# Kernel tuning notes

Measured on AMD Instinct MI355X. Metric: run time of the kernel, lower is better.

Reference implementation:

```python
import jax, jax.numpy as jnp
import numpy as np

NS = 100000   # state nodes
NM = 50000    # model nodes (== model_node_count == action space)
E = 600000    # edges
D = 128       # feature dim
HORIZON = 8
NEG_SLOPE = 0.2  # GATv2 default leaky_relu slope


def setup_inputs() -> dict:
    key = jax.random.key(0)
    ks = jax.random.split(key, 20)
    s = 1.0 / np.sqrt(D)
    state_features = jax.random.normal(ks[0], (NS, D), dtype=jnp.float32)
    model_features = jax.random.normal(ks[1], (NM, D), dtype=jnp.float32)
    src = jax.random.randint(ks[2], (E,), 0, NS)
    dst = jax.random.randint(ks[3], (E,), 0, NM)
    edge_index = jnp.stack([src, dst]).astype(jnp.int64)
    # GATv2Conv params (heads=1)
    W_l = jax.random.normal(ks[4], (D, D), dtype=jnp.float32) * s   # lin_l (src/state)
    W_r = jax.random.normal(ks[5], (D, D), dtype=jnp.float32) * s   # lin_r (dst/model)
    att = jax.random.normal(ks[6], (D,), dtype=jnp.float32) * s
    conv_bias = jnp.zeros((D,), dtype=jnp.float32)
    # LSTMCell params (torch gate order i,f,g,o)
    lstm_Wih = jax.random.normal(ks[7], (4 * D, D), dtype=jnp.float32) * s
    lstm_Whh = jax.random.normal(ks[8], (4 * D, D), dtype=jnp.float32) * s
    lstm_bih = jnp.zeros((4 * D,), dtype=jnp.float32)
    lstm_bhh = jnp.zeros((4 * D,), dtype=jnp.float32)
    # predictor MLP: Linear(D,D) -> ReLU -> Linear(D, NM)
    pred_W1 = jax.random.normal(ks[9], (D, D), dtype=jnp.float32) * s
    pred_b1 = jnp.zeros((D,), dtype=jnp.float32)
    pred_W2 = jax.random.normal(ks[10], (NM, D), dtype=jnp.float32) * s
    pred_b2 = jnp.zeros((NM,), dtype=jnp.float32)
    # action embedding
    emb = jax.random.normal(ks[11], (NM, D), dtype=jnp.float32)
    return {
        'state_features': state_features, 'model_features': model_features,
        'edge_index': edge_index, 'W_l': W_l, 'W_r': W_r, 'att': att,
        'conv_bias': conv_bias, 'lstm_Wih': lstm_Wih, 'lstm_Whh': lstm_Whh,
        'lstm_bih': lstm_bih, 'lstm_bhh': lstm_bhh, 'pred_W1': pred_W1,
        'pred_b1': pred_b1, 'pred_W2': pred_W2, 'pred_b2': pred_b2, 'emb': emb,
    }


def _gatv2(state_features, model_features, edge_index, W_l, W_r, att, conv_bias):
    src, dst = edge_index[0], edge_index[1]
    x_l = state_features @ W_l.T        # [NS, D]
    x_r = model_features @ W_r.T        # [NM, D]
    # per-edge GATv2 score: a^T LeakyReLU(x_l[src] + x_r[dst])
    z = x_l[src] + x_r[dst]             # [E, D]
    e = jnp.where(z > 0, z, NEG_SLOPE * z) @ att  # [E]
    # scatter-softmax over destination segments
    m = jax.ops.segment_max(e, dst, num_segments=NM)
    ex = jnp.exp(e - m[dst])
    s = jax.ops.segment_sum(ex, dst, num_segments=NM)
    alpha = ex / s[dst]                 # [E]
    out = jax.ops.segment_sum(alpha[:, None] * x_l[src], dst, num_segments=NM)
    return out + conv_bias              # [NM, D]


def reference(state_features, model_features, edge_index, W_l, W_r, att,
              conv_bias, lstm_Wih, lstm_Whh, lstm_bih, lstm_bhh,
              pred_W1, pred_b1, pred_W2, pred_b2, emb):
    updated = _gatv2(state_features, model_features, edge_index, W_l, W_r, att, conv_bias)
    g = updated.mean(axis=0)            # global model feature [D]

    keys = jax.random.split(jax.random.key(42), HORIZON)

    def step(carry, key):
        h, c, inp = carry
        gates = inp @ lstm_Wih.T + lstm_bih + h @ lstm_Whh.T + lstm_bhh
        i, f, gg, o = jnp.split(gates, 4)
        i = jax.nn.sigmoid(i); f = jax.nn.sigmoid(f)
        gg = jnp.tanh(gg); o = jax.nn.sigmoid(o)
        c = f * c + i * gg
        h = o * jnp.tanh(c)
        logits = jax.nn.relu(h @ pred_W1.T + pred_b1) @ pred_W2.T + pred_b2
        action = jax.random.categorical(key, logits)
        log_prob = jax.nn.log_softmax(logits)[action]
        return (h, c, emb[action]), (action, log_prob)

    h0 = jnp.zeros((D,), dtype=state_features.dtype)
    c0 = jnp.zeros((D,), dtype=state_features.dtype)
    (h, c, _), (actions, log_probs) = jax.lax.scan(step, (h0, c0, g), keys)
    return actions, log_probs, h, c
```

## Files before the change

kernel.cpp:

```cpp
#include <hip/hip_runtime.h>

#define D 128

typedef short s16x8 __attribute__((ext_vector_type(8)));
typedef float f32x4 __attribute__((ext_vector_type(4)));


__device__ __forceinline__ unsigned int encf(float f) {
  unsigned int u = __float_as_uint(f);
  return (u & 0x80000000u) ? ~u : (u | 0x80000000u);
}
__device__ __forceinline__ unsigned short f2bf(float f) {
  unsigned int u = __float_as_uint(f);
  u += 0x7FFFu + ((u >> 16) & 1u);
  return (unsigned short)(u >> 16);
}
__device__ __forceinline__ float bf_lo(unsigned int u) {
  return __uint_as_float(u << 16);
}
__device__ __forceinline__ float bf_hi(unsigned int u) {
  return __uint_as_float(u & 0xFFFF0000u);
}

__device__ __forceinline__ void tf2x32(unsigned int k0, unsigned int k1,
                                       unsigned int& x0, unsigned int& x1) {
  unsigned int ks[3] = {k0, k1, k0 ^ k1 ^ 0x1BD11BDAu};
  x0 += ks[0]; x1 += ks[1];
  const unsigned int rotA[4] = {13u, 15u, 26u, 6u};
  const unsigned int rotB[4] = {17u, 29u, 16u, 24u};
#pragma unroll
  for (int g = 0; g < 5; ++g) {
    const unsigned int* rot = (g & 1) ? rotB : rotA;
#pragma unroll
    for (int i = 0; i < 4; ++i) {
      x0 += x1;
      x1 = (x1 << rot[i]) | (x1 >> (32u - rot[i]));
      x1 ^= x0;
    }
    x0 += ks[(g + 1) % 3];
    x1 += ks[(g + 2) % 3] + (unsigned int)(g + 1);
  }
}


__global__ __launch_bounds__(256) void norm_edges(const int* __restrict__ ei,
                                                  int* __restrict__ src32,
                                                  int* __restrict__ dst32,
                                                  int ne, int ns, int nm) {
  __shared__ int is64;
  if (threadIdx.x == 0) {
    int any = 0;
    for (int i = 1; i < 256; i += 2) any |= ei[i];
    is64 = (any == 0);
  }
  __syncthreads();
  int flag = is64;
  for (int i = blockIdx.x * 256 + threadIdx.x; i < ne; i += gridDim.x * 256) {
    int s = flag ? ei[2 * i] : ei[i];
    int d = flag ? ei[2 * ne + 2 * i] : ei[ne + i];
    s = s < 0 ? 0 : (s >= ns ? ns - 1 : s);
    d = d < 0 ? 0 : (d >= nm ? nm - 1 : d);
    src32[i] = s;
    dst32[i] = d;
  }
}


__device__ __forceinline__ int swz(int row, int kb) {
  return row * 256 + (kb ^ ((row & 7) << 4));
}

__global__ __launch_bounds__(256) void gemm_bf16(const float* __restrict__ X,
                                                 const float* __restrict__ W,
                                                 unsigned short* __restrict__ Y,
                                                 int N) {
  __shared__ __align__(16) unsigned short As[128 * 128];
  __shared__ __align__(16) unsigned short Bs[128 * 128];
  const int tid = threadIdx.x;
  const long long r0 = (long long)blockIdx.x * 128;

#pragma unroll 4
  for (int i = 0; i < 16; ++i) {
    int f = i * 256 + tid;
    int row = f >> 5;
    int j = f & 31;
    float4 wv = *(const float4*)(W + row * D + j * 4);
    uint2 wp;
    wp.x = (unsigned int)f2bf(wv.x) | ((unsigned int)f2bf(wv.y) << 16);
    wp.y = (unsigned int)f2bf(wv.z) | ((unsigned int)f2bf(wv.w) << 16);
    *(uint2*)((char*)Bs + swz(row, j * 8)) = wp;
    long long rr = r0 + row;
    if (rr >= N) rr = N - 1;
    float4 xv = *(const float4*)(X + rr * D + j * 4);
    uint2 xp;
    xp.x = (unsigned int)f2bf(xv.x) | ((unsigned int)f2bf(xv.y) << 16);
    xp.y = (unsigned int)f2bf(xv.z) | ((unsigned int)f2bf(xv.w) << 16);
    *(uint2*)((char*)As + swz(row, j * 8)) = xp;
  }
  __syncthreads();

  const int lane = tid & 63;
  const int wid = tid >> 6;
  const int wr = wid >> 1;
  const int wc = wid & 1;
  const int cl = lane & 15;
  const int sub = lane >> 4;

  f32x4 acc[4][4] = {};

#pragma unroll
  for (int ks = 0; ks < 4; ++ks) {
    s16x8 av[4], bv[4];
#pragma unroll
    for (int m = 0; m < 4; ++m)
      av[m] = *(const s16x8*)((const char*)As +
                              swz(wr * 64 + m * 16 + cl, ks * 64 + sub * 16));
#pragma unroll
    for (int n = 0; n < 4; ++n)
      bv[n] = *(const s16x8*)((const char*)Bs +
                              swz(wc * 64 + n * 16 + cl, ks * 64 + sub * 16));
#pragma unroll
    for (int m = 0; m < 4; ++m)
#pragma unroll
      for (int n = 0; n < 4; ++n)
        acc[m][n] = __builtin_amdgcn_mfma_f32_16x16x32_bf16(av[m], bv[n],
                                                            acc[m][n], 0, 0, 0);
  }

#pragma unroll
  for (int m = 0; m < 4; ++m) {
#pragma unroll
    for (int j = 0; j < 4; ++j) {
      long long row = r0 + wr * 64 + m * 16 + sub * 4 + j;
      if (row < N) {
        unsigned short* yp = Y + row * D + wc * 64 + cl;
#pragma unroll
        for (int n = 0; n < 4; ++n) yp[n * 16] = f2bf(acc[m][n][j]);
      }
    }
  }
}


__global__ __launch_bounds__(256) void edge_scores(
    const unsigned short* __restrict__ xlh, const unsigned short* __restrict__ xrh,
    const int* __restrict__ src, const int* __restrict__ dst,
    const float* __restrict__ att, float* __restrict__ e_ex,
    float* __restrict__ s_sum, int ne) {
  int tid = threadIdx.x;
  int lane = tid & 63;
  int q = lane & 15;
  int sub = lane >> 4;
  int wid = (blockIdx.x * 256 + tid) >> 6;
  int nw = (gridDim.x * 256) >> 6;
  float4 a0 = ((const float4*)att)[2 * q];
  float4 a1 = ((const float4*)att)[2 * q + 1];
  for (int e0 = wid * 8; e0 < ne; e0 += nw * 8) {
    int eA = e0 + sub, eB = e0 + 4 + sub;
    int okA = eA < ne, okB = eB < ne;
    int sA = okA ? src[eA] : 0, dA = okA ? dst[eA] : 0;
    int sB = okB ? src[eB] : 0, dB = okB ? dst[eB] : 0;
    uint4 lA = *(const uint4*)(xlh + (long long)sA * D + q * 8);
    uint4 rA = *(const uint4*)(xrh + (long long)dA * D + q * 8);
    uint4 lB = *(const uint4*)(xlh + (long long)sB * D + q * 8);
    uint4 rB = *(const uint4*)(xrh + (long long)dB * D + q * 8);
    float z, vA = 0.f, vB = 0.f;
    z = bf_lo(lA.x) + bf_lo(rA.x); vA += (z > 0.f ? z : 0.2f * z) * a0.x;
    z = bf_hi(lA.x) + bf_hi(rA.x); vA += (z > 0.f ? z : 0.2f * z) * a0.y;
    z = bf_lo(lA.y) + bf_lo(rA.y); vA += (z > 0.f ? z : 0.2f * z) * a0.z;
    z = bf_hi(lA.y) + bf_hi(rA.y); vA += (z > 0.f ? z : 0.2f * z) * a0.w;
    z = bf_lo(lA.z) + bf_lo(rA.z); vA += (z > 0.f ? z : 0.2f * z) * a1.x;
    z = bf_hi(lA.z) + bf_hi(rA.z); vA += (z > 0.f ? z : 0.2f * z) * a1.y;
    z = bf_lo(lA.w) + bf_lo(rA.w); vA += (z > 0.f ? z : 0.2f * z) * a1.z;
    z = bf_hi(lA.w) + bf_hi(rA.w); vA += (z > 0.f ? z : 0.2f * z) * a1.w;
    z = bf_lo(lB.x) + bf_lo(rB.x); vB += (z > 0.f ? z : 0.2f * z) * a0.x;
    z = bf_hi(lB.x) + bf_hi(rB.x); vB += (z > 0.f ? z : 0.2f * z) * a0.y;
    z = bf_lo(lB.y) + bf_lo(rB.y); vB += (z > 0.f ? z : 0.2f * z) * a0.z;
    z = bf_hi(lB.y) + bf_hi(rB.y); vB += (z > 0.f ? z : 0.2f * z) * a0.w;
    z = bf_lo(lB.z) + bf_lo(rB.z); vB += (z > 0.f ? z : 0.2f * z) * a1.x;
    z = bf_hi(lB.z) + bf_hi(rB.z); vB += (z > 0.f ? z : 0.2f * z) * a1.y;
    z = bf_lo(lB.w) + bf_lo(rB.w); vB += (z > 0.f ? z : 0.2f * z) * a1.z;
    z = bf_hi(lB.w) + bf_hi(rB.w); vB += (z > 0.f ? z : 0.2f * z) * a1.w;
#pragma unroll
    for (int o = 8; o > 0; o >>= 1) vA += __shfl_xor(vA, o, 64);
#pragma unroll
    for (int o = 8; o > 0; o >>= 1) vB += __shfl_xor(vB, o, 64);
    if (q == 0) {
      if (okA) { float ex = expf(vA); e_ex[eA] = ex; atomicAdd(&s_sum[dA], ex); }
      if (okB) { float ex = expf(vB); e_ex[eB] = ex; atomicAdd(&s_sum[dB], ex); }
    }
  }
}


__global__ __launch_bounds__(256) void edge_coef(
    const float* __restrict__ e_ex, const int* __restrict__ src,
    const int* __restrict__ dst, const float* __restrict__ s_sum,
    float* __restrict__ coef, int ne) {
  int i = blockIdx.x * 256 + threadIdx.x;
  if (i < ne) {
    float w = e_ex[i] / s_sum[dst[i]];
    atomicAdd(&coef[src[i]], w);
  }
}


__global__ __launch_bounds__(256) void weighted_sum(
    const unsigned short* __restrict__ xlh, const float* __restrict__ coef,
    float* __restrict__ g_vec, int ns) {
  __shared__ float red[4][D];
  int lane = threadIdx.x & 63;
  int wv = threadIdx.x >> 6;
  int wid = blockIdx.x * 4 + wv;
  int nw = gridDim.x * 4;
  float ax = 0.f, ay = 0.f;
  for (int s = wid; s < ns; s += nw) {
    float w = coef[s];
    unsigned int x2 = ((const unsigned int*)(xlh + (long long)s * D))[lane];
    ax += w * bf_lo(x2);
    ay += w * bf_hi(x2);
  }
  red[wv][2 * lane] = ax;
  red[wv][2 * lane + 1] = ay;
  __syncthreads();
  if (threadIdx.x < D) {
    float t = red[0][threadIdx.x] + red[1][threadIdx.x] + red[2][threadIdx.x] +
              red[3][threadIdx.x];
    atomicAdd(&g_vec[threadIdx.x], t);
  }
}


__global__ __launch_bounds__(256) void lstm_gates(
    const float* __restrict__ g_vec, const float* __restrict__ conv_bias,
    const float* __restrict__ Wih, const float* __restrict__ Whh,
    const float* __restrict__ bih, const float* __restrict__ bhh,
    const float* __restrict__ emb, const float* __restrict__ logits,
    const unsigned long long* __restrict__ amax,
    const float* __restrict__ sumexp, const float* __restrict__ st_h,
    float* __restrict__ st_gates, float* __restrict__ out, int nm, float nmf,
    int t) {
  __shared__ float vin[D], hprev[D];
  const int tid = threadIdx.x;

  int a = 0;
  if (t > 0) {
    unsigned long long p = amax[t - 1];
    a = (int)(0xFFFFFFFFu - (unsigned int)(p & 0xFFFFFFFFull));
    a = a < 0 ? 0 : (a >= nm ? nm - 1 : a);
  }
  if (t > 0 && blockIdx.x == 0 && tid == 0) {
    out[t - 1] = (float)a;
    out[8 + t - 1] = logits[a] - logf(sumexp[t - 1]);
  }
  if (tid < D) {
    vin[tid] = (t == 0) ? (g_vec[tid] / nmf + conv_bias[tid])
                        : emb[(long long)a * D + tid];
    hprev[tid] = (t == 0) ? 0.f : st_h[tid];
  }
  __syncthreads();

  int r = blockIdx.x * 16 + (tid >> 4);
  int q = tid & 15;
  const float4* wi = (const float4*)(Wih + (long long)r * D + q * 8);
  const float4* wh = (const float4*)(Whh + (long long)r * D + q * 8);
  float4 a0 = wi[0], a1 = wi[1];
  float4 b0 = wh[0], b1 = wh[1];
  int kb = q * 8;
  float s = a0.x * vin[kb] + a0.y * vin[kb + 1] + a0.z * vin[kb + 2] +
            a0.w * vin[kb + 3] + a1.x * vin[kb + 4] + a1.y * vin[kb + 5] +
            a1.z * vin[kb + 6] + a1.w * vin[kb + 7] + b0.x * hprev[kb] +
            b0.y * hprev[kb + 1] + b0.z * hprev[kb + 2] + b0.w * hprev[kb + 3] +
            b1.x * hprev[kb + 4] + b1.y * hprev[kb + 5] + b1.z * hprev[kb + 6] +
            b1.w * hprev[kb + 7];
  s += __shfl_xor(s, 1, 64);
  s += __shfl_xor(s, 2, 64);
  s += __shfl_xor(s, 4, 64);
  s += __shfl_xor(s, 8, 64);
  if (q == 0) st_gates[r] = s + bih[r] + bhh[r];
}


__global__ __launch_bounds__(256) void logits_fused2(
    const float* __restrict__ st_gates, const float* __restrict__ W1,
    const float* __restrict__ b1, const float* __restrict__ W2,
    const float* __restrict__ b2, float* __restrict__ st_c,
    float* __restrict__ st_h, float* __restrict__ logits,
    unsigned long long* __restrict__ amax, float* __restrict__ sumexp,
    int nm, int t) {
  __shared__ float hn_s[D];
  __shared__ float hid_s[D];
  __shared__ unsigned long long pkw[4];
  __shared__ float exw[4];
  const int tid = threadIdx.x;
  const int bid = blockIdx.x;

  if (tid < D) {
    float gi = st_gates[tid], gf = st_gates[D + tid],
          gg = st_gates[2 * D + tid], go = st_gates[3 * D + tid];
    float i_ = 1.f / (1.f + expf(-gi));
    float f_ = 1.f / (1.f + expf(-gf));
    float g_ = tanhf(gg);
    float o_ = 1.f / (1.f + expf(-go));
    float cprev = (t == 0) ? 0.f : st_c[((t & 1) ^ 1) * D + tid];
    float cn = f_ * cprev + i_ * g_;
    float hn = o_ * tanhf(cn);
    hn_s[tid] = hn;
    if (bid == 0) {
      st_c[(t & 1) * D + tid] = cn;
      st_h[tid] = hn;
    }
  }
  __syncthreads();

  if (tid < D) {
    const float4* w = (const float4*)(W1 + tid * D);
    float s0 = 0.f, s1 = 0.f, s2 = 0.f, s3 = 0.f;
#pragma unroll 8
    for (int k = 0; k < 32; ++k) {
      float4 ww = w[k];
      s0 += ww.x * hn_s[4 * k];
      s1 += ww.y * hn_s[4 * k + 1];
      s2 += ww.z * hn_s[4 * k + 2];
      s3 += ww.w * hn_s[4 * k + 3];
    }
    hid_s[tid] = fmaxf(((s0 + s1) + (s2 + s3)) + b1[tid], 0.f);
  }
  __syncthreads();

  int row = bid * 64 + (tid >> 2);
  int q = tid & 3;
  float ex = 0.f;
  unsigned long long pk = 0ull;
  if (row < nm) {
    const float4* w = (const float4*)(W2 + (long long)row * D + q * 32);
    float s0 = 0.f, s1 = 0.f, s2 = 0.f, s3 = 0.f;
#pragma unroll
    for (int k = 0; k < 8; ++k) {
      float4 ww = w[k];
      int kb = q * 32 + 4 * k;
      s0 += ww.x * hid_s[kb];
      s1 += ww.y * hid_s[kb + 1];
      s2 += ww.z * hid_s[kb + 2];
      s3 += ww.w * hid_s[kb + 3];
    }
    float s = (s0 + s1) + (s2 + s3);
    s += __shfl_xor(s, 1, 64);
    s += __shfl_xor(s, 2, 64);
    if (q == 0) {
      float lv = s + b2[row];
      logits[row] = lv;
      ex = expf(lv);
      unsigned int k0 = 0u, k1 = (unsigned int)t;
      tf2x32(0u, 42u, k0, k1);
      unsigned int x0 = 0u, x1 = (unsigned int)row;
      tf2x32(k0, k1, x0, x1);
      unsigned int bits = x0 ^ x1;
      float f = __uint_as_float((bits >> 9) | 0x3f800000u) - 1.0f;
      const float tiny = 1.1754943508222875e-38f;
      float u = fmaxf(tiny, f * (1.0f - tiny) + tiny);
      float gmb = -logf(-logf(u));
      float pert = lv + gmb;
      pk = ((unsigned long long)encf(pert) << 32) |
           (unsigned long long)(0xFFFFFFFFu - (unsigned int)row);
    }
  }
#pragma unroll
  for (int o = 32; o > 0; o >>= 1) {
    unsigned long long pko = __shfl_xor(pk, o, 64);
    pk = pko > pk ? pko : pk;
    ex += __shfl_xor(ex, o, 64);
  }
  int wv = tid >> 6;
  if ((tid & 63) == 0) {
    pkw[wv] = pk;
    exw[wv] = ex;
  }
  __syncthreads();
  if (tid == 0) {
    unsigned long long pm = pkw[0];
    pm = pkw[1] > pm ? pkw[1] : pm;
    pm = pkw[2] > pm ? pkw[2] : pm;
    pm = pkw[3] > pm ? pkw[3] : pm;
    atomicMax(&amax[t], pm);
    atomicAdd(&sumexp[t], ((exw[0] + exw[1]) + (exw[2] + exw[3])));
  }
}


__global__ __launch_bounds__(128) void final_out(
    const float* __restrict__ h, const float* __restrict__ c,
    const float* __restrict__ logits, const unsigned long long* __restrict__ amax,
    const float* __restrict__ sumexp, float* __restrict__ out, int nm) {
  int tid = threadIdx.x;
  if (tid == 0) {
    unsigned long long p = amax[7];
    int a = (int)(0xFFFFFFFFu - (unsigned int)(p & 0xFFFFFFFFull));
    a = a < 0 ? 0 : (a >= nm ? nm - 1 : a);
    out[7] = (float)a;
    out[15] = logits[a] - logf(sumexp[7]);
  }
  out[16 + tid] = h[tid];
  out[144 + tid] = c[tid];
}


extern "C" void kernel_launch(void* const* d_in, const int* in_sizes, int n_in,
                              void* d_out, int out_size, void* d_ws, size_t ws_size,
                              hipStream_t stream) {
  const float* state_features = (const float*)d_in[0];
  const float* model_features = (const float*)d_in[1];
  const int* edge_index = (const int*)d_in[2];
  const float* W_l = (const float*)d_in[3];
  const float* W_r = (const float*)d_in[4];
  const float* att = (const float*)d_in[5];
  const float* conv_bias = (const float*)d_in[6];
  const float* Wih = (const float*)d_in[7];
  const float* Whh = (const float*)d_in[8];
  const float* bih = (const float*)d_in[9];
  const float* bhh = (const float*)d_in[10];
  const float* W1 = (const float*)d_in[11];
  const float* b1 = (const float*)d_in[12];
  const float* W2 = (const float*)d_in[13];
  const float* b2 = (const float*)d_in[14];
  const float* emb = (const float*)d_in[15];
  float* out = (float*)d_out;

  const int NS = in_sizes[0] / D;
  const int NM = in_sizes[1] / D;
  const int E = in_sizes[2] / 2;

  char* ws = (char*)d_ws;
  size_t off = 0;
  auto alloc = [&](size_t bytes) -> void* {
    void* p = ws + off;
    off = (off + bytes + 255) & ~(size_t)255;
    return p;
  };
  unsigned short* xlh = (unsigned short*)alloc((size_t)NS * D * 2);
  unsigned short* xrh = (unsigned short*)alloc((size_t)NM * D * 2);
  float* e_ex = (float*)alloc((size_t)E * 4);
  int* src32 = (int*)alloc((size_t)E * 4);
  int* dst32 = (int*)alloc((size_t)E * 4);
  float* logits = (float*)alloc((size_t)NM * 4);
  float* st_h = (float*)alloc(D * 4);
  float* st_c = (float*)alloc(2 * D * 4);
  float* st_gates = (float*)alloc(4 * D * 4);
  size_t zstart = off;
  float* s_sum = (float*)alloc((size_t)NM * 4);
  float* coef = (float*)alloc((size_t)NS * 4);
  float* g_vec = (float*)alloc(D * 4);
  float* st_sumexp = (float*)alloc(8 * 4);
  unsigned long long* st_amax = (unsigned long long*)alloc(8 * 8);
  size_t zend = off;

  hipMemsetAsync(ws + zstart, 0, zend - zstart, stream);

  norm_edges<<<512, 256, 0, stream>>>(edge_index, src32, dst32, E, NS, NM);

  gemm_bf16<<<(NS + 127) / 128, 256, 0, stream>>>(state_features, W_l, xlh, NS);
  gemm_bf16<<<(NM + 127) / 128, 256, 0, stream>>>(model_features, W_r, xrh, NM);

  edge_scores<<<2048, 256, 0, stream>>>(xlh, xrh, src32, dst32, att, e_ex,
                                        s_sum, E);
  edge_coef<<<(E + 255) / 256, 256, 0, stream>>>(e_ex, src32, dst32, s_sum,
                                                 coef, E);
  weighted_sum<<<1024, 256, 0, stream>>>(xlh, coef, g_vec, NS);

  int nb2 = (NM + 63) / 64;
  for (int t = 0; t < 8; ++t) {
    lstm_gates<<<32, 256, 0, stream>>>(g_vec, conv_bias, Wih, Whh, bih, bhh,
                                       emb, logits, st_amax, st_sumexp, st_h,
                                       st_gates, out, NM, (float)NM, t);
    logits_fused2<<<nb2, 256, 0, stream>>>(st_gates, W1, b1, W2, b2, st_c,
                                           st_h, logits, st_amax, st_sumexp,
                                           NM, t);
  }

  final_out<<<1, 128, 0, stream>>>(st_h, st_c + D, logits, st_amax, st_sumexp,
                                   out, NM);
}
```

Baseline: 503.4 us.

## Fold edge normalization into consumers, merge GEMMs, persist logits grid

Removes the norm_edges kernel and its src32/dst32 buffers, so edge_scores and edge_coef read edge_index directly, detecting int64 layout with a wave ballot and clamping inline. The two bf16 projection GEMMs become one persistent 256-block kernel that loops over the tiles of both matrices. logits_fused3 uses a grid-stride loop over 256 blocks, accumulating the max and sum per thread before reducing, which cuts the number of blocks and atomics per step. Grid sizes for edge and weighted-sum kernels are also reduced. The cost is re-reading 64-bit indices twice and less parallelism in the GEMM and logits kernels.

```diff
diff --git a/kernel.cpp b/kernel.cpp
--- a/kernel.cpp
+++ b/kernel.cpp
@@ -42,27 +42,12 @@
   }
 }
 
-
-__global__ __launch_bounds__(256) void norm_edges(const int* __restrict__ ei,
-                                                  int* __restrict__ src32,
-                                                  int* __restrict__ dst32,
-                                                  int ne, int ns, int nm) {
-  __shared__ int is64;
-  if (threadIdx.x == 0) {
-    int any = 0;
-    for (int i = 1; i < 256; i += 2) any |= ei[i];
-    is64 = (any == 0);
-  }
-  __syncthreads();
-  int flag = is64;
-  for (int i = blockIdx.x * 256 + threadIdx.x; i < ne; i += gridDim.x * 256) {
-    int s = flag ? ei[2 * i] : ei[i];
-    int d = flag ? ei[2 * ne + 2 * i] : ei[ne + i];
-    s = s < 0 ? 0 : (s >= ns ? ns - 1 : s);
-    d = d < 0 ? 0 : (d >= nm ? nm - 1 : d);
-    src32[i] = s;
-    dst32[i] = d;
-  }
+__device__ __forceinline__ int detect64(const int* ei) {
+  int v = 0;
+  int tid = threadIdx.x;
+  if (tid < 64) v = ei[2 * tid + 1];
+  unsigned long long b = __ballot(v != 0);
+  return b == 0ull;
 }
 
 
@@ -70,72 +55,87 @@
   return row * 256 + (kb ^ ((row & 7) << 4));
 }
 
-__global__ __launch_bounds__(256) void gemm_bf16(const float* __restrict__ X,
-                                                 const float* __restrict__ W,
-                                                 unsigned short* __restrict__ Y,
-                                                 int N) {
+__global__ __launch_bounds__(256) void gemm_bf16_all(
+    const float* __restrict__ Xs, const float* __restrict__ Wl,
+    unsigned short* __restrict__ Ys, int NSn, const float* __restrict__ Xm,
+    const float* __restrict__ Wr, unsigned short* __restrict__ Ym, int NMn) {
   __shared__ __align__(16) unsigned short As[128 * 128];
   __shared__ __align__(16) unsigned short Bs[128 * 128];
   const int tid = threadIdx.x;
-  const long long r0 = (long long)blockIdx.x * 128;
+  const int nsb = (NSn + 127) >> 7;
+  const int nmb = (NMn + 127) >> 7;
+
+  for (int v = blockIdx.x; v < nsb + nmb; v += gridDim.x) {
+    const float* X;
+    const float* W;
+    unsigned short* Y;
+    int N;
+    long long r0;
+    if (v < nsb) {
+      X = Xs; W = Wl; Y = Ys; N = NSn; r0 = (long long)v * 128;
+    } else {
+      X = Xm; W = Wr; Y = Ym; N = NMn; r0 = (long long)(v - nsb) * 128;
+    }
+    __syncthreads();
 
 #pragma unroll 4
-  for (int i = 0; i < 16; ++i) {
-    int f = i * 256 + tid;
-    int row = f >> 5;
-    int j = f & 31;
-    float4 wv = *(const float4*)(W + row * D + j * 4);
-    uint2 wp;
-    wp.x = (unsigned int)f2bf(wv.x) | ((unsigned int)f2bf(wv.y) << 16);
-    wp.y = (unsigned int)f2bf(wv.z) | ((unsigned int)f2bf(wv.w) << 16);
-    *(uint2*)((char*)Bs + swz(row, j * 8)) = wp;
-    long long rr = r0 + row;
-    if (rr >= N) rr = N - 1;
-    float4 xv = *(const float4*)(X + rr * D + j * 4);
-    uint2 xp;
-    xp.x = (unsigned int)f2bf(xv.x) | ((unsigned int)f2bf(xv.y) << 16);
-    xp.y = (unsigned int)f2bf(xv.z) | ((unsigned int)f2bf(xv.w) << 16);
-    *(uint2*)((char*)As + swz(row, j * 8)) = xp;
-  }
-  __syncthreads();
-
-  const int lane = tid & 63;
-  const int wid = tid >> 6;
-  const int wr = wid >> 1;
-  const int wc = wid & 1;
-  const int cl = lane & 15;
-  const int sub = lane >> 4;
-
-  f32x4 acc[4][4] = {};
-
-#pragma unroll
-  for (int ks = 0; ks < 4; ++ks) {
-    s16x8 av[4], bv[4];
-#pragma unroll
-    for (int m = 0; m < 4; ++m)
-      av[m] = *(const s16x8*)((const char*)As +
-                              swz(wr * 64 + m * 16 + cl, ks * 64 + sub * 16));
-#pragma unroll
-    for (int n = 0; n < 4; ++n)
-      bv[n] = *(const s16x8*)((const char*)Bs +
-                              swz(wc * 64 + n * 16 + cl, ks * 64 + sub * 16));
-#pragma unroll
-    for (int m = 0; m < 4; ++m)
+    for (int i = 0; i < 16; ++i) {
+      int f = i * 256 + tid;
+      int row = f >> 5;
+      int j = f & 31;
+      float4 wv = *(const float4*)(W + row * D + j * 4);
+      uint2 wp;
+      wp.x = (unsigned int)f2bf(wv.x) | ((unsigned int)f2bf(wv.y) << 16);
+      wp.y = (unsigned int)f2bf(wv.z) | ((unsigned int)f2bf(wv.w) << 16);
+      *(uint2*)((char*)Bs + swz(row, j * 8)) = wp;
+      long long rr = r0 + row;
+      if (rr >= N) rr = N - 1;
+      float4 xv = *(const float4*)(X + rr * D + j * 4);
+      uint2 xp;
+      xp.x = (unsigned int)f2bf(xv.x) | ((unsigned int)f2bf(xv.y) << 16);
+      xp.y = (unsigned int)f2bf(xv.z) | ((unsigned int)f2bf(xv.w) << 16);
+      *(uint2*)((char*)As + swz(row, j * 8)) = xp;
+    }
+    __syncthreads();
+
+    const int lane = tid & 63;
+    const int wid = tid >> 6;
+    const int wr = wid >> 1;
+    const int wc = wid & 1;
+    const int cl = lane & 15;
+    const int sub = lane >> 4;
+
+    f32x4 acc[4][4] = {};
+
+#pragma unroll
+    for (int ks = 0; ks < 4; ++ks) {
+      s16x8 av[4], bv[4];
+#pragma unroll
+      for (int m = 0; m < 4; ++m)
+        av[m] = *(const s16x8*)((const char*)As +
+                                swz(wr * 64 + m * 16 + cl, ks * 64 + sub * 16));
 #pragma unroll
       for (int n = 0; n < 4; ++n)
-        acc[m][n] = __builtin_amdgcn_mfma_f32_16x16x32_bf16(av[m], bv[n],
-                                                            acc[m][n], 0, 0, 0);
-  }
-
-#pragma unroll
-  for (int m = 0; m < 4; ++m) {
-#pragma unroll
-    for (int j = 0; j < 4; ++j) {
-      long long row = r0 + wr * 64 + m * 16 + sub * 4 + j;
-      if (row < N) {
-        unsigned short* yp = Y + row * D + wc * 64 + cl;
-#pragma unroll
-        for (int n = 0; n < 4; ++n) yp[n * 16] = f2bf(acc[m][n][j]);
+        bv[n] = *(const s16x8*)((const char*)Bs +
+                                swz(wc * 64 + n * 16 + cl, ks * 64 + sub * 16));
+#pragma unroll
+      for (int m = 0; m < 4; ++m)
+#pragma unroll
+        for (int n = 0; n < 4; ++n)
+          acc[m][n] = __builtin_amdgcn_mfma_f32_16x16x32_bf16(av[m], bv[n],
+                                                              acc[m][n], 0, 0, 0);
+    }
+
+#pragma unroll
+    for (int m = 0; m < 4; ++m) {
+#pragma unroll
+      for (int j = 0; j < 4; ++j) {
+        long long row = r0 + wr * 64 + m * 16 + sub * 4 + j;
+        if (row < N) {
+          unsigned short* yp = Y + row * D + wc * 64 + cl;
+#pragma unroll
+          for (int n = 0; n < 4; ++n) yp[n * 16] = f2bf(acc[m][n][j]);
+        }
       }
     }
   }
@@ -144,10 +144,16 @@
 
 __global__ __launch_bounds__(256) void edge_scores(
     const unsigned short* __restrict__ xlh, const unsigned short* __restrict__ xrh,
-    const int* __restrict__ src, const int* __restrict__ dst,
-    const float* __restrict__ att, float* __restrict__ e_ex,
-    float* __restrict__ s_sum, int ne) {
+    const int* __restrict__ ei, const float* __restrict__ att,
+    float* __restrict__ e_ex, float* __restrict__ s_sum, int ne, int ns,
+    int nm) {
+  __shared__ int f64s;
   int tid = threadIdx.x;
+  int d64 = detect64(ei);
+  if (tid == 0) f64s = d64;
+  __syncthreads();
+  const int f64 = f64s;
+
   int lane = tid & 63;
   int q = lane & 15;
   int sub = lane >> 4;
@@ -158,8 +164,19 @@
   for (int e0 = wid * 8; e0 < ne; e0 += nw * 8) {
     int eA = e0 + sub, eB = e0 + 4 + sub;
     int okA = eA < ne, okB = eB < ne;
-    int sA = okA ? src[eA] : 0, dA = okA ? dst[eA] : 0;
-    int sB = okB ? src[eB] : 0, dB = okB ? dst[eB] : 0;
+    int sA = 0, dA = 0, sB = 0, dB = 0;
+    if (okA) {
+      sA = f64 ? ei[2 * eA] : ei[eA];
+      dA = f64 ? ei[2 * ne + 2 * eA] : ei[ne + eA];
+      sA = sA < 0 ? 0 : (sA >= ns ? ns - 1 : sA);
+      dA = dA < 0 ? 0 : (dA >= nm ? nm - 1 : dA);
+    }
+    if (okB) {
+      sB = f64 ? ei[2 * eB] : ei[eB];
+      dB = f64 ? ei[2 * ne + 2 * eB] : ei[ne + eB];
+      sB = sB < 0 ? 0 : (sB >= ns ? ns - 1 : sB);
+      dB = dB < 0 ? 0 : (dB >= nm ? nm - 1 : dB);
+    }
     uint4 lA = *(const uint4*)(xlh + (long long)sA * D + q * 8);
     uint4 rA = *(const uint4*)(xrh + (long long)dA * D + q * 8);
     uint4 lB = *(const uint4*)(xlh + (long long)sB * D + q * 8);
@@ -194,13 +211,22 @@
 
 
 __global__ __launch_bounds__(256) void edge_coef(
-    const float* __restrict__ e_ex, const int* __restrict__ src,
-    const int* __restrict__ dst, const float* __restrict__ s_sum,
-    float* __restrict__ coef, int ne) {
-  int i = blockIdx.x * 256 + threadIdx.x;
-  if (i < ne) {
-    float w = e_ex[i] / s_sum[dst[i]];
-    atomicAdd(&coef[src[i]], w);
+    const float* __restrict__ e_ex, const int* __restrict__ ei,
+    const float* __restrict__ s_sum, float* __restrict__ coef, int ne, int ns,
+    int nm) {
+  __shared__ int f64s;
+  int tid = threadIdx.x;
+  int d64 = detect64(ei);
+  if (tid == 0) f64s = d64;
+  __syncthreads();
+  const int f64 = f64s;
+  for (int i = blockIdx.x * 256 + tid; i < ne; i += gridDim.x * 256) {
+    int s_ = f64 ? ei[2 * i] : ei[i];
+    int d_ = f64 ? ei[2 * ne + 2 * i] : ei[ne + i];
+    s_ = s_ < 0 ? 0 : (s_ >= ns ? ns - 1 : s_);
+    d_ = d_ < 0 ? 0 : (d_ >= nm ? nm - 1 : d_);
+    float w = e_ex[i] / s_sum[d_];
+    atomicAdd(&coef[s_], w);
   }
 }
 
@@ -281,7 +307,7 @@
 }
 
 
-__global__ __launch_bounds__(256) void logits_fused2(
+__global__ __launch_bounds__(256) void logits_fused3(
     const float* __restrict__ st_gates, const float* __restrict__ W1,
     const float* __restrict__ b1, const float* __restrict__ W2,
     const float* __restrict__ b2, float* __restrict__ st_c,
@@ -328,53 +354,57 @@
   }
   __syncthreads();
 
-  int row = bid * 64 + (tid >> 2);
-  int q = tid & 3;
-  float ex = 0.f;
-  unsigned long long pk = 0ull;
-  if (row < nm) {
-    const float4* w = (const float4*)(W2 + (long long)row * D + q * 32);
-    float s0 = 0.f, s1 = 0.f, s2 = 0.f, s3 = 0.f;
-#pragma unroll
-    for (int k = 0; k < 8; ++k) {
-      float4 ww = w[k];
-      int kb = q * 32 + 4 * k;
-      s0 += ww.x * hid_s[kb];
-      s1 += ww.y * hid_s[kb + 1];
-      s2 += ww.z * hid_s[kb + 2];
-      s3 += ww.w * hid_s[kb + 3];
-    }
-    float s = (s0 + s1) + (s2 + s3);
-    s += __shfl_xor(s, 1, 64);
-    s += __shfl_xor(s, 2, 64);
-    if (q == 0) {
-      float lv = s + b2[row];
-      logits[row] = lv;
-      ex = expf(lv);
-      unsigned int k0 = 0u, k1 = (unsigned int)t;
-      tf2x32(0u, 42u, k0, k1);
-      unsigned int x0 = 0u, x1 = (unsigned int)row;
-      tf2x32(k0, k1, x0, x1);
-      unsigned int bits = x0 ^ x1;
-      float f = __uint_as_float((bits >> 9) | 0x3f800000u) - 1.0f;
-      const float tiny = 1.1754943508222875e-38f;
-      float u = fmaxf(tiny, f * (1.0f - tiny) + tiny);
-      float gmb = -logf(-logf(u));
-      float pert = lv + gmb;
-      pk = ((unsigned long long)encf(pert) << 32) |
-           (unsigned long long)(0xFFFFFFFFu - (unsigned int)row);
+  unsigned int k0 = 0u, k1 = (unsigned int)t;
+  tf2x32(0u, 42u, k0, k1);
+
+  const int q = tid & 3;
+  float exacc = 0.f;
+  unsigned long long pkacc = 0ull;
+  for (int r0 = bid * 64; r0 < nm; r0 += gridDim.x * 64) {
+    int row = r0 + (tid >> 2);
+    if (row < nm) {
+      const float4* w = (const float4*)(W2 + (long long)row * D + q * 32);
+      float s0 = 0.f, s1 = 0.f, s2 = 0.f, s3 = 0.f;
+#pragma unroll
+      for (int k = 0; k < 8; ++k) {
+        float4 ww = w[k];
+        int kb = q * 32 + 4 * k;
+        s0 += ww.x * hid_s[kb];
+        s1 += ww.y * hid_s[kb + 1];
+        s2 += ww.z * hid_s[kb + 2];
+        s3 += ww.w * hid_s[kb + 3];
+      }
+      float s = (s0 + s1) + (s2 + s3);
+      s += __shfl_xor(s, 1, 64);
+      s += __shfl_xor(s, 2, 64);
+      if (q == 0) {
+        float lv = s + b2[row];
+        logits[row] = lv;
+        exacc += expf(lv);
+        unsigned int x0 = 0u, x1 = (unsigned int)row;
+        tf2x32(k0, k1, x0, x1);
+        unsigned int bits = x0 ^ x1;
+        float f = __uint_as_float((bits >> 9) | 0x3f800000u) - 1.0f;
+        const float tiny = 1.1754943508222875e-38f;
+        float u = fmaxf(tiny, f * (1.0f - tiny) + tiny);
+        float gmb = -logf(-logf(u));
+        float pert = lv + gmb;
+        unsigned long long pk = ((unsigned long long)encf(pert) << 32) |
+                                (unsigned long long)(0xFFFFFFFFu - (unsigned int)row);
+        pkacc = pk > pkacc ? pk : pkacc;
+      }
     }
   }
 #pragma unroll
   for (int o = 32; o > 0; o >>= 1) {
-    unsigned long long pko = __shfl_xor(pk, o, 64);
-    pk = pko > pk ? pko : pk;
-    ex += __shfl_xor(ex, o, 64);
+    unsigned long long pko = __shfl_xor(pkacc, o, 64);
+    pkacc = pko > pkacc ? pko : pkacc;
+    exacc += __shfl_xor(exacc, o, 64);
   }
   int wv = tid >> 6;
   if ((tid & 63) == 0) {
-    pkw[wv] = pk;
-    exw[wv] = ex;
+    pkw[wv] = pkacc;
+    exw[wv] = exacc;
   }
   __syncthreads();
   if (tid == 0) {
@@ -440,8 +470,6 @@
   unsigned short* xlh = (unsigned short*)alloc((size_t)NS * D * 2);
   unsigned short* xrh = (unsigned short*)alloc((size_t)NM * D * 2);
   float* e_ex = (float*)alloc((size_t)E * 4);
-  int* src32 = (int*)alloc((size_t)E * 4);
-  int* dst32 = (int*)alloc((size_t)E * 4);
   float* logits = (float*)alloc((size_t)NM * 4);
   float* st_h = (float*)alloc(D * 4);
   float* st_c = (float*)alloc(2 * D * 4);
@@ -456,23 +484,20 @@
 
   hipMemsetAsync(ws + zstart, 0, zend - zstart, stream);
 
-  norm_edges<<<512, 256, 0, stream>>>(edge_index, src32, dst32, E, NS, NM);
-
-  gemm_bf16<<<(NS + 127) / 128, 256, 0, stream>>>(state_features, W_l, xlh, NS);
-  gemm_bf16<<<(NM + 127) / 128, 256, 0, stream>>>(model_features, W_r, xrh, NM);
-
-  edge_scores<<<2048, 256, 0, stream>>>(xlh, xrh, src32, dst32, att, e_ex,
-                                        s_sum, E);
-  edge_coef<<<(E + 255) / 256, 256, 0, stream>>>(e_ex, src32, dst32, s_sum,
-                                                 coef, E);
-  weighted_sum<<<1024, 256, 0, stream>>>(xlh, coef, g_vec, NS);
-
-  int nb2 = (NM + 63) / 64;
+  gemm_bf16_all<<<256, 256, 0, stream>>>(state_features, W_l, xlh, NS,
+                                         model_features, W_r, xrh, NM);
+
+  edge_scores<<<1024, 256, 0, stream>>>(xlh, xrh, edge_index, att, e_ex,
+                                        s_sum, E, NS, NM);
+  edge_coef<<<1024, 256, 0, stream>>>(e_ex, edge_index, s_sum, coef, E, NS,
+                                      NM);
+  weighted_sum<<<512, 256, 0, stream>>>(xlh, coef, g_vec, NS);
+
   for (int t = 0; t < 8; ++t) {
     lstm_gates<<<32, 256, 0, stream>>>(g_vec, conv_bias, Wih, Whh, bih, bhh,
                                        emb, logits, st_amax, st_sumexp, st_h,
                                        st_gates, out, NM, (float)NM, t);
-    logits_fused2<<<nb2, 256, 0, stream>>>(st_gates, W1, b1, W2, b2, st_c,
+    logits_fused3<<<256, 256, 0, stream>>>(st_gates, W1, b1, W2, b2, st_c,
                                            st_h, logits, st_amax, st_sumexp,
                                            NM, t);
   }
```

Measured after the change: 420.6 us. 16.4% less time.
